# Kernel tuning notes

Measured on AMD Instinct MI355X. Metric: run time of the kernel, lower is better.

The kernel has to match this reference:

```python
import jax, jax.numpy as jnp
import numpy as np

E = 1024
H = 16
HD = E // H
FF = 4 * E
B, T = 2, 2048


def _linear_params(key, fan_in, fan_out):
    k1, k2 = jax.random.split(key)
    bound = 1.0 / np.sqrt(fan_in)
    W = jax.random.uniform(k1, (fan_out, fan_in), jnp.float32, -bound, bound)
    b = jax.random.uniform(k2, (fan_out,), jnp.float32, -bound, bound)
    return W, b


def setup_inputs() -> dict:
    key = jax.random.key(0)
    keys = jax.random.split(key, 8)
    x = jax.random.normal(keys[0], (B, T, E), jnp.float32)
    Wq, bq = _linear_params(keys[1], E, E)
    Wk, bk = _linear_params(keys[2], E, E)
    Wv, bv = _linear_params(keys[3], E, E)
    Wo, bo = _linear_params(keys[4], E, E)
    W1, b1 = _linear_params(keys[5], E, FF)
    W2, b2 = _linear_params(keys[6], FF, E)
    ln1_g = jnp.ones((E,), jnp.float32); ln1_b = jnp.zeros((E,), jnp.float32)
    ln2_g = jnp.ones((E,), jnp.float32); ln2_b = jnp.zeros((E,), jnp.float32)
    return {"x": x, "Wq": Wq, "bq": bq, "Wk": Wk, "bk": bk, "Wv": Wv, "bv": bv,
            "Wo": Wo, "bo": bo, "W1": W1, "b1": b1, "W2": W2, "b2": b2,
            "ln1_g": ln1_g, "ln1_b": ln1_b, "ln2_g": ln2_g, "ln2_b": ln2_b}


def _layernorm(x, g, b, eps=1e-5):
    mu = jnp.mean(x, axis=-1, keepdims=True)
    var = jnp.var(x, axis=-1, keepdims=True)
    return (x - mu) * jax.lax.rsqrt(var + eps) * g + b


def reference(x, Wq, bq, Wk, bk, Wv, bv, Wo, bo, W1, b1, W2, b2,
              ln1_g, ln1_b, ln2_g, ln2_b):
    Bc, Tc, Ec = x.shape
    h = _layernorm(x, ln1_g, ln1_b)
    # projections (torch Linear: y = x @ W.T + b)
    q = (h @ Wq.T + bq).reshape(Bc, Tc, H, HD).transpose(0, 2, 1, 3)  # [B,H,T,hd]
    k = (h @ Wk.T + bk).reshape(Bc, Tc, H, HD).transpose(0, 2, 1, 3)
    v = (h @ Wv.T + bv).reshape(Bc, Tc, H, HD).transpose(0, 2, 1, 3)
    scores = jnp.einsum('bhqd,bhkd->bhqk', q, k) / np.sqrt(HD).astype(np.float32)
    causal = jnp.tril(jnp.ones((Tc, Tc), bool))
    scores = jnp.where(causal, scores, -jnp.inf)
    att = jax.nn.softmax(scores, axis=-1)  # dropout = identity (eval)
    out = jnp.einsum('bhqk,bhkd->bhqd', att, v)
    out = out.transpose(0, 2, 1, 3).reshape(Bc, Tc, Ec)
    x = x + out @ Wo.T + bo
    h2 = _layernorm(x, ln2_g, ln2_b)
    ff = jax.nn.relu(h2 @ W1.T + b1) @ W2.T + b2
    return x + ff
```

## Files before the change

kernel.cpp:

```cpp
#include <hip/hip_runtime.h>

typedef unsigned short u16;
typedef __bf16 bf16x8 __attribute__((ext_vector_type(8)));
typedef float f32x4 __attribute__((ext_vector_type(4)));

#define E_ 1024
#define T_ 2048
#define B_ 2
#define H_ 16
#define FF_ 4096
#define M_ 4096

__device__ __forceinline__ u16 f2b(float f) {
    union { float f; unsigned u; } c; c.f = f;
    unsigned r = c.u + 0x7FFFu + ((c.u >> 16) & 1u);
    return (u16)(r >> 16);
}
__device__ __forceinline__ u16 f2bt(float f) {
    union { float f; unsigned u; } c; c.f = f;
    return (u16)(c.u >> 16);
}

__device__ __forceinline__ void gl16(const u16* g, u16* l) {
    __builtin_amdgcn_global_load_lds(
        (__attribute__((address_space(1))) void*)g,
        (__attribute__((address_space(3))) void*)l, 16, 0, 0);
}

template<int N> __device__ __forceinline__ void wait_vmcnt() {
    if constexpr (N == 2)      asm volatile("s_waitcnt vmcnt(2)" ::: "memory");
    else if constexpr (N == 3) asm volatile("s_waitcnt vmcnt(3)" ::: "memory");
    else if constexpr (N == 4) asm volatile("s_waitcnt vmcnt(4)" ::: "memory");
    else                       asm volatile("s_waitcnt vmcnt(0)" ::: "memory");
}

__global__ __launch_bounds__(256) void cvt_ln(
        const float* __restrict__ Wq, const float* __restrict__ Wk,
        const float* __restrict__ Wv, const float* __restrict__ Wo,
        const float* __restrict__ W1, const float* __restrict__ W2,
        const float* __restrict__ bq, const float* __restrict__ bk,
        const float* __restrict__ bv,
        u16* __restrict__ WqkvB, u16* __restrict__ WoB,
        u16* __restrict__ W1B, u16* __restrict__ W2B,
        float* __restrict__ bqkv,
        const float* __restrict__ x, const float* __restrict__ g1,
        const float* __restrict__ b1v, u16* __restrict__ hB) {
    if (blockIdx.x < 1024) {
        int row = blockIdx.x * 4 + (threadIdx.x >> 6);
        int t = threadIdx.x & 63;
        const float* xr = x + (size_t)row * E_;
        float v[16];
        float sum = 0.f, ss = 0.f;
#pragma unroll
        for (int c = 0; c < 4; c++) {
            float4 f = *(const float4*)&xr[c * 256 + t * 4];
            v[c * 4 + 0] = f.x; v[c * 4 + 1] = f.y; v[c * 4 + 2] = f.z; v[c * 4 + 3] = f.w;
            sum += f.x + f.y + f.z + f.w;
            ss += f.x * f.x + f.y * f.y + f.z * f.z + f.w * f.w;
        }
#pragma unroll
        for (int d = 32; d; d >>= 1) {
            sum += __shfl_xor(sum, d);
            ss  += __shfl_xor(ss, d);
        }
        float mu = sum * (1.f / E_);
        float var = ss * (1.f / E_) - mu * mu;
        float rs = rsqrtf(var + 1e-5f);
#pragma unroll
        for (int c = 0; c < 4; c++) {
            int idx = c * 256 + t * 4;
            float4 g4 = *(const float4*)&g1[idx];
            float4 b4 = *(const float4*)&b1v[idx];
            ushort4 o;
            o.x = f2b((v[c * 4 + 0] - mu) * rs * g4.x + b4.x);
            o.y = f2b((v[c * 4 + 1] - mu) * rs * g4.y + b4.y);
            o.z = f2b((v[c * 4 + 2] - mu) * rs * g4.z + b4.z);
            o.w = f2b((v[c * 4 + 3] - mu) * rs * g4.w + b4.w);
            *(ushort4*)&hB[(size_t)row * E_ + idx] = o;
        }
        return;
    }
    int i = (blockIdx.x - 1024) * 256 + threadIdx.x;
    if (i >= 3146496) return;
    if (i >= 3145728) {
        int j = i - 3145728;
        const float* s = (j < 256) ? bq : (j < 512) ? bk : bv;
        int jj = j & 255;
        *(float4*)&bqkv[j * 4] = *(const float4*)&s[jj * 4];
        return;
    }
    const float* src; u16* dst; int j;
    if (i < 786432) {
        src = (i < 262144) ? Wq : (i < 524288) ? Wk : Wv;
        j = i & 262143;
        dst = WqkvB + (i >> 18) * (E_ * E_);
    } else if (i < 1048576) { j = i - 786432;  src = Wo; dst = WoB; }
    else if (i < 2097152)   { j = i - 1048576; src = W1; dst = W1B; }
    else                    { j = i - 2097152; src = W2; dst = W2B; }
    float4 f = *(const float4*)&src[j * 4];
    ushort4 o;
    o.x = f2b(f.x); o.y = f2b(f.y); o.z = f2b(f.z); o.w = f2b(f.w);
    *(ushort4*)&dst[j * 4] = o;
}

__global__ __launch_bounds__(64) void ln_fwd(u16* __restrict__ out, const float* __restrict__ x,
                                             const float* __restrict__ g, const float* __restrict__ bta) {
    int row = blockIdx.x;
    int t = threadIdx.x;
    const float* xr = x + (size_t)row * E_;
    float v[16];
    float sum = 0.f, ss = 0.f;
#pragma unroll
    for (int c = 0; c < 4; c++) {
        float4 f = *(const float4*)&xr[c * 256 + t * 4];
        v[c * 4 + 0] = f.x; v[c * 4 + 1] = f.y; v[c * 4 + 2] = f.z; v[c * 4 + 3] = f.w;
        sum += f.x + f.y + f.z + f.w;
        ss += f.x * f.x + f.y * f.y + f.z * f.z + f.w * f.w;
    }
#pragma unroll
    for (int d = 32; d; d >>= 1) {
        sum += __shfl_xor(sum, d);
        ss  += __shfl_xor(ss, d);
    }
    float mu = sum * (1.f / E_);
    float var = ss * (1.f / E_) - mu * mu;
    float rs = rsqrtf(var + 1e-5f);
#pragma unroll
    for (int c = 0; c < 4; c++) {
        int idx = c * 256 + t * 4;
        float4 g4 = *(const float4*)&g[idx];
        float4 b4 = *(const float4*)&bta[idx];
        ushort4 o;
        o.x = f2b((v[c * 4 + 0] - mu) * rs * g4.x + b4.x);
        o.y = f2b((v[c * 4 + 1] - mu) * rs * g4.y + b4.y);
        o.z = f2b((v[c * 4 + 2] - mu) * rs * g4.z + b4.z);
        o.w = f2b((v[c * 4 + 3] - mu) * rs * g4.w + b4.w);
        *(ushort4*)&out[(size_t)row * E_ + idx] = o;
    }
}

template<int BM, int BN, int BUFS>
__global__ __launch_bounds__(256) void gemm_bt(
        const u16* __restrict__ A, const u16* __restrict__ Bt,
        const float* __restrict__ bias, const float* __restrict__ residual,
        float* __restrict__ outF, float* __restrict__ oP1,
        float* __restrict__ oP2, float* __restrict__ oP3,
        u16* __restrict__ outB, u16* __restrict__ outVt,
        int M, int N, int K, int ldk, int relu, int qkvmode, int swz) {
    constexpr int MT = BM / 32, NT = BN / 32;
    constexpr int LA = BM / 64, LB = BN / 64;
    __shared__ __align__(16) u16 As[BUFS][BM * 32];
    __shared__ __align__(16) u16 Bs[BUFS][BN * 32];
    int tid = threadIdx.x;
    int bx = blockIdx.x, by = blockIdx.y;
    if (swz) {
        int gx = gridDim.x;
        int nwg = gx * gridDim.y;
        int lin = by * gx + bx;
        int wv = (lin & 7) * (nwg >> 3) + (lin >> 3);
        bx = wv % gx; by = wv / gx;
    }
    int m0 = by * BM, n0 = bx * BN;
    int kz = blockIdx.z;
    int koff = kz * K;
    int wave = tid >> 6, lane = tid & 63;
    int wm = wave & 1, wn = wave >> 1;
    int r16 = lane & 15, kg = lane >> 4;

    const u16* gA = A + (size_t)(m0 + wave * (BM / 4) + (lane >> 2)) * ldk + koff + (lane & 3) * 8;
    const u16* gB = Bt + (size_t)(n0 + wave * (BN / 4) + (lane >> 2)) * ldk + koff + (lane & 3) * 8;
    size_t row16 = (size_t)16 * ldk;
    int aoff = wave * (BM / 4) * 32;
    int boff = wave * (BN / 4) * 32;

    f32x4 acc[MT][NT] = {};

    const int nk = K >> 5;

    auto issue = [&](int kt, int buf) {
        int k1 = kt << 5;
        gl16(gA + k1, As[buf] + aoff);
        if (LA == 2) gl16(gA + k1 + row16, As[buf] + aoff + 512);
        gl16(gB + k1, Bs[buf] + boff);
        if (LB == 2) gl16(gB + k1 + row16, Bs[buf] + boff + 512);
    };

    auto compute = [&](int cb) {
        bf16x8 af[MT], bfr[NT];
#pragma unroll
        for (int mt = 0; mt < MT; mt++)
            af[mt] = *(const bf16x8*)&As[cb][(wm * (BM / 2) + mt * 16 + r16) * 32 + kg * 8];
#pragma unroll
        for (int nt = 0; nt < NT; nt++)
            bfr[nt] = *(const bf16x8*)&Bs[cb][(wn * (BN / 2) + nt * 16 + r16) * 32 + kg * 8];
#pragma unroll
        for (int mt = 0; mt < MT; mt++)
#pragma unroll
            for (int nt = 0; nt < NT; nt++)
                acc[mt][nt] = __builtin_amdgcn_mfma_f32_16x16x32_bf16(af[mt], bfr[nt], acc[mt][nt], 0, 0, 0);
    };

    if constexpr (BUFS == 2) {
        issue(0, 0);
        for (int ks = 0; ks < nk; ks++) {
            __syncthreads();
            if (ks + 1 < nk) issue(ks + 1, (ks + 1) & 1);
            compute(ks & 1);
        }
    } else {
        issue(0, 0);
        issue(1, 1);
        int cur = 0;
        for (int ks = 0; ks < nk - 1; ks++) {
            wait_vmcnt<LA + LB>();
            __builtin_amdgcn_s_barrier();
            asm volatile("" ::: "memory");
            if (ks + 2 < nk) {
                int p2 = cur ? cur - 1 : 2;
                issue(ks + 2, p2);
            }
            compute(cur);
            cur = (cur < 2) ? cur + 1 : 0;
        }
        asm volatile("s_waitcnt vmcnt(0)" ::: "memory");
        __builtin_amdgcn_s_barrier();
        asm volatile("" ::: "memory");
        compute(cur);
    }

#pragma unroll
    for (int mt = 0; mt < MT; mt++) {
#pragma unroll
        for (int nt = 0; nt < NT; nt++) {
            int gm = m0 + wm * (BM / 2) + mt * 16 + kg * 4;
            int gn = n0 + wn * (BN / 2) + nt * 16 + r16;
            float bv = bias[gn];
            if (qkvmode) {
                if (gn < 2048) {
                    float scl = (gn < 1024) ? 0.18033688f : 1.0f;
#pragma unroll
                    for (int r = 0; r < 4; r++)
                        outB[(size_t)(gm + r) * 2048 + gn] = f2b((acc[mt][nt][r] + bv) * scl);
                } else {
                    int bq_ = gm >> 11, tq = gm & 2047, d = gn - 2048;
                    ushort4 ov;
                    ov.x = f2b(acc[mt][nt][0] + bv);
                    ov.y = f2b(acc[mt][nt][1] + bv);
                    ov.z = f2b(acc[mt][nt][2] + bv);
                    ov.w = f2b(acc[mt][nt][3] + bv);
                    *(ushort4*)&outVt[((size_t)(bq_ * 1024 + d)) * 2048 + tq] = ov;
                }
            } else if (oP1) {
                float* po = (kz == 1) ? oP1 : (kz == 2) ? oP2 : oP3;
#pragma unroll
                for (int r = 0; r < 4; r++) {
                    size_t off = (size_t)(gm + r) * N + gn;
                    if (kz == 0) {
                        float v = acc[mt][nt][r] + bv;
                        if (residual) v += residual[off];
                        outF[off] = v;
                    } else {
                        po[off] = acc[mt][nt][r];
                    }
                }
            } else {
#pragma unroll
                for (int r = 0; r < 4; r++) {
                    float v = acc[mt][nt][r] + bv;
                    size_t off = (size_t)(gm + r) * N + gn;
                    if (residual) v += residual[off];
                    if (relu) v = fmaxf(v, 0.f);
                    if (outF) outF[off] = v;
                    else outB[off] = f2b(v);
                }
            }
        }
    }
}

__global__ __launch_bounds__(256) void addf3(float* __restrict__ d, const float* __restrict__ a,
                                             const float* __restrict__ b, const float* __restrict__ c) {
    size_t i = ((size_t)blockIdx.x * 256 + threadIdx.x) * 4;
    float4 vd = *(float4*)&d[i];
    float4 va = *(const float4*)&a[i];
    float4 vb = *(const float4*)&b[i];
    float4 vc = *(const float4*)&c[i];
    vd.x += va.x + vb.x + vc.x;
    vd.y += va.y + vb.y + vc.y;
    vd.z += va.z + vb.z + vc.z;
    vd.w += va.w + vb.w + vc.w;
    *(float4*)&d[i] = vd;
}

#define AST 68
__global__ __launch_bounds__(256) void attn_mfma(
        const u16* __restrict__ qk, const u16* __restrict__ vt,
        u16* __restrict__ out) {
    __shared__ __align__(16) u16 Ks[2][64 * AST];
    __shared__ __align__(16) u16 Vs[2][64 * AST];
    __shared__ __align__(16) u16 Ps[4][16 * AST];

    int bz = blockIdx.x;
    int h  = bz & 15;
    int b  = (bz >> 4) & 1;
    int qt = bz >> 5;

    int tid = threadIdx.x;
    int w = tid >> 6, lane = tid & 63;
    int g = lane >> 4, l16 = lane & 15;

    int qrow = qt * 64 + w * 16 + l16;
    bf16x8 qf[2];
    qf[0] = *(const bf16x8*)&qk[(size_t)(b * T_ + qrow) * 2048 + h * 64 + g * 8];
    qf[1] = *(const bf16x8*)&qk[(size_t)(b * T_ + qrow) * 2048 + h * 64 + 32 + g * 8];

    f32x4 o[4] = {};
    f32x4 lp = {0.f, 0.f, 0.f, 0.f};

    int r1 = tid >> 3, col1 = (tid & 7) * 8;
    const u16* gK = qk + (size_t)(b * T_) * 2048 + 1024 + h * 64;
    const u16* gV = vt + (size_t)(b * 1024 + h * 64) * 2048;

    uint4 kr1 = *(const uint4*)&gK[(size_t)r1 * 2048 + col1];
    uint4 kr2 = *(const uint4*)&gK[(size_t)(r1 + 32) * 2048 + col1];
    uint4 vr1 = *(const uint4*)&gV[(size_t)r1 * 2048 + col1];
    uint4 vr2 = *(const uint4*)&gV[(size_t)(r1 + 32) * 2048 + col1];

    for (int t = 0; t <= qt; t++) {
        int cur = t & 1;
        *(uint4*)&Ks[cur][r1 * AST + col1] = kr1;
        *(uint4*)&Ks[cur][(r1 + 32) * AST + col1] = kr2;
        *(uint4*)&Vs[cur][r1 * AST + col1] = vr1;
        *(uint4*)&Vs[cur][(r1 + 32) * AST + col1] = vr2;
        __syncthreads();
        if (t < qt) {
            int j1 = (t + 1) * 64;
            kr1 = *(const uint4*)&gK[(size_t)(j1 + r1) * 2048 + col1];
            kr2 = *(const uint4*)&gK[(size_t)(j1 + r1 + 32) * 2048 + col1];
            vr1 = *(const uint4*)&gV[(size_t)r1 * 2048 + j1 + col1];
            vr2 = *(const uint4*)&gV[(size_t)(r1 + 32) * 2048 + j1 + col1];
        }

        f32x4 s[4];
#pragma unroll
        for (int nt = 0; nt < 4; nt++) {
            f32x4 c16 = {-16.f, -16.f, -16.f, -16.f};
            bf16x8 k0 = *(const bf16x8*)&Ks[cur][(nt * 16 + l16) * AST + g * 8];
            bf16x8 k1 = *(const bf16x8*)&Ks[cur][(nt * 16 + l16) * AST + 32 + g * 8];
            s[nt] = __builtin_amdgcn_mfma_f32_16x16x32_bf16(qf[0], k0, c16, 0, 0, 0);
            s[nt] = __builtin_amdgcn_mfma_f32_16x16x32_bf16(qf[1], k1, s[nt], 0, 0, 0);
        }

        if (t == qt) {
            int j0 = t * 64;
#pragma unroll
            for (int nt = 0; nt < 4; nt++) {
                int key = j0 + nt * 16 + l16;
#pragma unroll
                for (int r = 0; r < 4; r++) {
                    int q = qt * 64 + w * 16 + g * 4 + r;
                    if (key > q) s[nt][r] = -INFINITY;
                }
            }
        }

#pragma unroll
        for (int nt = 0; nt < 4; nt++)
#pragma unroll
            for (int r = 0; r < 4; r++) {
                float p = exp2f(s[nt][r]);
                lp[r] += p;
                Ps[w][(g * 4 + r) * AST + nt * 16 + l16] = f2bt(p);
            }

#pragma unroll
        for (int kf = 0; kf < 2; kf++) {
            bf16x8 pf = *(const bf16x8*)&Ps[w][l16 * AST + kf * 32 + g * 8];
#pragma unroll
            for (int nt = 0; nt < 4; nt++) {
                bf16x8 vf = *(const bf16x8*)&Vs[cur][(nt * 16 + l16) * AST + kf * 32 + g * 8];
                o[nt] = __builtin_amdgcn_mfma_f32_16x16x32_bf16(pf, vf, o[nt], 0, 0, 0);
            }
        }
    }

#pragma unroll
    for (int x = 1; x <= 8; x <<= 1)
#pragma unroll
        for (int r = 0; r < 4; r++)
            lp[r] += __shfl_xor(lp[r], x);

    float inv[4];
#pragma unroll
    for (int r = 0; r < 4; r++) inv[r] = 1.f / lp[r];
    int qg = qt * 64 + w * 16 + g * 4;
#pragma unroll
    for (int nt = 0; nt < 4; nt++)
#pragma unroll
        for (int r = 0; r < 4; r++)
            out[(size_t)(b * T_ + qg + r) * E_ + h * 64 + nt * 16 + l16] =
                f2b(o[nt][r] * inv[r]);
}

extern "C" void kernel_launch(void* const* d_in, const int* in_sizes, int n_in,
                              void* d_out, int out_size, void* d_ws, size_t ws_size,
                              hipStream_t stream) {
    const float* x    = (const float*)d_in[0];
    const float* Wq   = (const float*)d_in[1];
    const float* bq   = (const float*)d_in[2];
    const float* Wk   = (const float*)d_in[3];
    const float* bk   = (const float*)d_in[4];
    const float* Wv   = (const float*)d_in[5];
    const float* bv   = (const float*)d_in[6];
    const float* Wo   = (const float*)d_in[7];
    const float* bo   = (const float*)d_in[8];
    const float* W1   = (const float*)d_in[9];
    const float* b1   = (const float*)d_in[10];
    const float* W2   = (const float*)d_in[11];
    const float* b2   = (const float*)d_in[12];
    const float* ln1g = (const float*)d_in[13];
    const float* ln1b = (const float*)d_in[14];
    const float* ln2g = (const float*)d_in[15];
    const float* ln2b = (const float*)d_in[16];

    char* ws = (char*)d_ws;
    size_t off = 0;
    auto alloc = [&](size_t bytes) { char* p = ws + off; off += (bytes + 255) & ~(size_t)255; return p; };

    u16*   hB    = (u16*)  alloc((size_t)M_ * E_ * 2);
    u16*   WqkvB = (u16*)  alloc((size_t)3 * E_ * E_ * 2);
    u16*   WoB   = (u16*)  alloc((size_t)E_ * E_ * 2);
    u16*   W1B   = (u16*)  alloc((size_t)FF_ * E_ * 2);
    u16*   W2B   = (u16*)  alloc((size_t)E_ * FF_ * 2);
    float* bqkv  = (float*)alloc(3 * E_ * 4);
    u16*   qkB   = (u16*)  alloc((size_t)M_ * 2 * E_ * 2);
    u16*   vtG   = (u16*)  alloc((size_t)M_ * E_ * 2);
    u16*   attnB = (u16*)  alloc((size_t)M_ * E_ * 2);
    float* x2    = (float*)alloc((size_t)M_ * E_ * 4);
    u16*   h2B   = (u16*)  alloc((size_t)M_ * E_ * 2);
    u16*   rB    = (u16*)  alloc((size_t)M_ * FF_ * 2);
    float* P1    = (float*)alloc((size_t)M_ * E_ * 4);
    float* P2 = (float*)qkB;
    float* P3 = (float*)ws;

    cvt_ln<<<1024 + 12291, 256, 0, stream>>>(Wq, Wk, Wv, Wo, W1, W2, bq, bk, bv,
                                             WqkvB, WoB, W1B, W2B, bqkv,
                                             x, ln1g, ln1b, hB);

    gemm_bt<128, 128, 2><<<dim3(3 * E_ / 128, M_ / 128), 256, 0, stream>>>(
        hB, WqkvB, bqkv, nullptr, nullptr, nullptr, nullptr, nullptr, qkB, vtG,
        M_, 3 * E_, E_, E_, 0, 1, 0);

    attn_mfma<<<B_ * H_ * (T_ / 64), 256, 0, stream>>>(qkB, vtG, attnB);

    gemm_bt<64, 128, 2><<<dim3(E_ / 128, M_ / 64), 256, 0, stream>>>(
        attnB, WoB, bo, x, x2, nullptr, nullptr, nullptr, nullptr, nullptr,
        M_, E_, E_, E_, 0, 0, 0);

    ln_fwd<<<M_, 64, 0, stream>>>(h2B, x2, ln2g, ln2b);

    gemm_bt<128, 128, 2><<<dim3(FF_ / 128, M_ / 128), 256, 0, stream>>>(
        h2B, W1B, b1, nullptr, nullptr, nullptr, nullptr, nullptr, rB, nullptr,
        M_, FF_, E_, E_, 1, 0, 1);

    gemm_bt<128, 128, 2><<<dim3(E_ / 128, M_ / 128, 4), 256, 0, stream>>>(
        rB, W2B, b2, x2, (float*)d_out, P1, P2, P3, nullptr, nullptr,
        M_, E_, FF_ / 4, FF_, 0, 0, 1);

    addf3<<<(M_ * E_) / (256 * 4), 256, 0, stream>>>((float*)d_out, P1, P2, P3);
}
```

Before: 389.1 us.

## Double attention query tile per block and halve FFN2 split-K factor

The attention kernel now has each block handle 128 query rows, with each wave computing two 16-row sub-tiles. Each K/V tile loaded into shared memory is therefore reused twice, and the grid shrinks to half as many blocks. Separately, the second FFN GEMM drops from split-K 4 to split-K 2, so only one partial buffer has to be reduced by a simpler add kernel. The trade-offs are fewer blocks, which makes causal load imbalance worse, a larger register footprint in attention, and lower parallelism in the W2 GEMM.

```diff
diff --git a/kernel.cpp b/kernel.cpp
--- a/kernel.cpp
+++ b/kernel.cpp
@@ -278,18 +278,12 @@
     }
 }
 
-__global__ __launch_bounds__(256) void addf3(float* __restrict__ d, const float* __restrict__ a,
-                                             const float* __restrict__ b, const float* __restrict__ c) {
+__global__ __launch_bounds__(256) void addf1(float* __restrict__ d, const float* __restrict__ p) {
     size_t i = ((size_t)blockIdx.x * 256 + threadIdx.x) * 4;
-    float4 vd = *(float4*)&d[i];
-    float4 va = *(const float4*)&a[i];
-    float4 vb = *(const float4*)&b[i];
-    float4 vc = *(const float4*)&c[i];
-    vd.x += va.x + vb.x + vc.x;
-    vd.y += va.y + vb.y + vc.y;
-    vd.z += va.z + vb.z + vc.z;
-    vd.w += va.w + vb.w + vc.w;
-    *(float4*)&d[i] = vd;
+    float4 a = *(float4*)&d[i];
+    float4 b = *(const float4*)&p[i];
+    a.x += b.x; a.y += b.y; a.z += b.z; a.w += b.w;
+    *(float4*)&d[i] = a;
 }
 
 #define AST 68
@@ -298,24 +292,28 @@
         u16* __restrict__ out) {
     __shared__ __align__(16) u16 Ks[2][64 * AST];
     __shared__ __align__(16) u16 Vs[2][64 * AST];
-    __shared__ __align__(16) u16 Ps[4][16 * AST];
+    __shared__ __align__(16) u16 Ps[4][32 * AST];
 
     int bz = blockIdx.x;
     int h  = bz & 15;
     int b  = (bz >> 4) & 1;
-    int qt = bz >> 5;
+    int q0 = bz >> 5;
 
     int tid = threadIdx.x;
     int w = tid >> 6, lane = tid & 63;
     int g = lane >> 4, l16 = lane & 15;
 
-    int qrow = qt * 64 + w * 16 + l16;
-    bf16x8 qf[2];
-    qf[0] = *(const bf16x8*)&qk[(size_t)(b * T_ + qrow) * 2048 + h * 64 + g * 8];
-    qf[1] = *(const bf16x8*)&qk[(size_t)(b * T_ + qrow) * 2048 + h * 64 + 32 + g * 8];
-
-    f32x4 o[4] = {};
-    f32x4 lp = {0.f, 0.f, 0.f, 0.f};
+    int qbase = q0 * 128 + w * 32;
+    bf16x8 qf[2][2];
+#pragma unroll
+    for (int s = 0; s < 2; s++) {
+        const u16* qp = &qk[(size_t)(b * T_ + qbase + s * 16 + l16) * 2048 + h * 64];
+        qf[s][0] = *(const bf16x8*)&qp[g * 8];
+        qf[s][1] = *(const bf16x8*)&qp[32 + g * 8];
+    }
+
+    f32x4 o[2][4] = {};
+    f32x4 lp[2] = {};
 
     int r1 = tid >> 3, col1 = (tid & 7) * 8;
     const u16* gK = qk + (size_t)(b * T_) * 2048 + 1024 + h * 64;
@@ -326,14 +324,15 @@
     uint4 vr1 = *(const uint4*)&gV[(size_t)r1 * 2048 + col1];
     uint4 vr2 = *(const uint4*)&gV[(size_t)(r1 + 32) * 2048 + col1];
 
-    for (int t = 0; t <= qt; t++) {
+    const int ntiles = 2 * q0 + 2;
+    for (int t = 0; t < ntiles; t++) {
         int cur = t & 1;
         *(uint4*)&Ks[cur][r1 * AST + col1] = kr1;
         *(uint4*)&Ks[cur][(r1 + 32) * AST + col1] = kr2;
         *(uint4*)&Vs[cur][r1 * AST + col1] = vr1;
         *(uint4*)&Vs[cur][(r1 + 32) * AST + col1] = vr2;
         __syncthreads();
-        if (t < qt) {
+        if (t + 1 < ntiles) {
             int j1 = (t + 1) * 64;
             kr1 = *(const uint4*)&gK[(size_t)(j1 + r1) * 2048 + col1];
             kr2 = *(const uint4*)&gK[(size_t)(j1 + r1 + 32) * 2048 + col1];
@@ -341,65 +340,78 @@
             vr2 = *(const uint4*)&gV[(size_t)(r1 + 32) * 2048 + j1 + col1];
         }
 
-        f32x4 s[4];
-#pragma unroll
-        for (int nt = 0; nt < 4; nt++) {
-            f32x4 c16 = {-16.f, -16.f, -16.f, -16.f};
-            bf16x8 k0 = *(const bf16x8*)&Ks[cur][(nt * 16 + l16) * AST + g * 8];
-            bf16x8 k1 = *(const bf16x8*)&Ks[cur][(nt * 16 + l16) * AST + 32 + g * 8];
-            s[nt] = __builtin_amdgcn_mfma_f32_16x16x32_bf16(qf[0], k0, c16, 0, 0, 0);
-            s[nt] = __builtin_amdgcn_mfma_f32_16x16x32_bf16(qf[1], k1, s[nt], 0, 0, 0);
-        }
-
-        if (t == qt) {
-            int j0 = t * 64;
+        const bool diag = (t >= 2 * q0);
+        int j0 = t * 64;
+
+#pragma unroll
+        for (int s = 0; s < 2; s++) {
+            f32x4 sc[4];
 #pragma unroll
             for (int nt = 0; nt < 4; nt++) {
-                int key = j0 + nt * 16 + l16;
+                f32x4 c16 = {-16.f, -16.f, -16.f, -16.f};
+                bf16x8 k0 = *(const bf16x8*)&Ks[cur][(nt * 16 + l16) * AST + g * 8];
+                bf16x8 k1 = *(const bf16x8*)&Ks[cur][(nt * 16 + l16) * AST + 32 + g * 8];
+                sc[nt] = __builtin_amdgcn_mfma_f32_16x16x32_bf16(qf[s][0], k0, c16, 0, 0, 0);
+                sc[nt] = __builtin_amdgcn_mfma_f32_16x16x32_bf16(qf[s][1], k1, sc[nt], 0, 0, 0);
+            }
+
+            if (diag) {
+#pragma unroll
+                for (int nt = 0; nt < 4; nt++) {
+                    int key = j0 + nt * 16 + l16;
+#pragma unroll
+                    for (int r = 0; r < 4; r++) {
+                        int q = qbase + s * 16 + g * 4 + r;
+                        if (key > q) sc[nt][r] = -INFINITY;
+                    }
+                }
+            }
+
+#pragma unroll
+            for (int nt = 0; nt < 4; nt++)
 #pragma unroll
                 for (int r = 0; r < 4; r++) {
-                    int q = qt * 64 + w * 16 + g * 4 + r;
-                    if (key > q) s[nt][r] = -INFINITY;
+                    float p = exp2f(sc[nt][r]);
+                    lp[s][r] += p;
+                    Ps[w][(s * 16 + g * 4 + r) * AST + nt * 16 + l16] = f2bt(p);
+                }
+        }
+
+#pragma unroll
+        for (int s = 0; s < 2; s++) {
+#pragma unroll
+            for (int kf = 0; kf < 2; kf++) {
+                bf16x8 pf = *(const bf16x8*)&Ps[w][(s * 16 + l16) * AST + kf * 32 + g * 8];
+#pragma unroll
+                for (int nt = 0; nt < 4; nt++) {
+                    bf16x8 vf = *(const bf16x8*)&Vs[cur][(nt * 16 + l16) * AST + kf * 32 + g * 8];
+                    o[s][nt] = __builtin_amdgcn_mfma_f32_16x16x32_bf16(pf, vf, o[s][nt], 0, 0, 0);
                 }
             }
         }
-
+    }
+
+#pragma unroll
+    for (int s = 0; s < 2; s++)
+#pragma unroll
+        for (int x = 1; x <= 8; x <<= 1)
+#pragma unroll
+            for (int r = 0; r < 4; r++)
+                lp[s][r] += __shfl_xor(lp[s][r], x);
+
+#pragma unroll
+    for (int s = 0; s < 2; s++) {
+        float inv[4];
+#pragma unroll
+        for (int r = 0; r < 4; r++) inv[r] = 1.f / lp[s][r];
+        int qg = qbase + s * 16 + g * 4;
 #pragma unroll
         for (int nt = 0; nt < 4; nt++)
 #pragma unroll
-            for (int r = 0; r < 4; r++) {
-                float p = exp2f(s[nt][r]);
-                lp[r] += p;
-                Ps[w][(g * 4 + r) * AST + nt * 16 + l16] = f2bt(p);
-            }
-
-#pragma unroll
-        for (int kf = 0; kf < 2; kf++) {
-            bf16x8 pf = *(const bf16x8*)&Ps[w][l16 * AST + kf * 32 + g * 8];
-#pragma unroll
-            for (int nt = 0; nt < 4; nt++) {
-                bf16x8 vf = *(const bf16x8*)&Vs[cur][(nt * 16 + l16) * AST + kf * 32 + g * 8];
-                o[nt] = __builtin_amdgcn_mfma_f32_16x16x32_bf16(pf, vf, o[nt], 0, 0, 0);
-            }
-        }
-    }
-
-#pragma unroll
-    for (int x = 1; x <= 8; x <<= 1)
-#pragma unroll
-        for (int r = 0; r < 4; r++)
-            lp[r] += __shfl_xor(lp[r], x);
-
-    float inv[4];
-#pragma unroll
-    for (int r = 0; r < 4; r++) inv[r] = 1.f / lp[r];
-    int qg = qt * 64 + w * 16 + g * 4;
-#pragma unroll
-    for (int nt = 0; nt < 4; nt++)
-#pragma unroll
-        for (int r = 0; r < 4; r++)
-            out[(size_t)(b * T_ + qg + r) * E_ + h * 64 + nt * 16 + l16] =
-                f2b(o[nt][r] * inv[r]);
+            for (int r = 0; r < 4; r++)
+                out[(size_t)(b * T_ + qg + r) * E_ + h * 64 + nt * 16 + l16] =
+                    f2b(o[s][nt][r] * inv[r]);
+    }
 }
 
 extern "C" void kernel_launch(void* const* d_in, const int* in_sizes, int n_in,
@@ -440,8 +452,6 @@
     u16*   h2B   = (u16*)  alloc((size_t)M_ * E_ * 2);
     u16*   rB    = (u16*)  alloc((size_t)M_ * FF_ * 2);
     float* P1    = (float*)alloc((size_t)M_ * E_ * 4);
-    float* P2 = (float*)qkB;
-    float* P3 = (float*)ws;
 
     cvt_ln<<<1024 + 12291, 256, 0, stream>>>(Wq, Wk, Wv, Wo, W1, W2, bq, bk, bv,
                                              WqkvB, WoB, W1B, W2B, bqkv,
@@ -451,7 +461,7 @@
         hB, WqkvB, bqkv, nullptr, nullptr, nullptr, nullptr, nullptr, qkB, vtG,
         M_, 3 * E_, E_, E_, 0, 1, 0);
 
-    attn_mfma<<<B_ * H_ * (T_ / 64), 256, 0, stream>>>(qkB, vtG, attnB);
+    attn_mfma<<<B_ * H_ * (T_ / 128), 256, 0, stream>>>(qkB, vtG, attnB);
 
     gemm_bt<64, 128, 2><<<dim3(E_ / 128, M_ / 64), 256, 0, stream>>>(
         attnB, WoB, bo, x, x2, nullptr, nullptr, nullptr, nullptr, nullptr,
@@ -463,9 +473,9 @@
         h2B, W1B, b1, nullptr, nullptr, nullptr, nullptr, nullptr, rB, nullptr,
         M_, FF_, E_, E_, 1, 0, 1);
 
-    gemm_bt<128, 128, 2><<<dim3(E_ / 128, M_ / 128, 4), 256, 0, stream>>>(
-        rB, W2B, b2, x2, (float*)d_out, P1, P2, P3, nullptr, nullptr,
-        M_, E_, FF_ / 4, FF_, 0, 0, 1);
-
-    addf3<<<(M_ * E_) / (256 * 4), 256, 0, stream>>>((float*)d_out, P1, P2, P3);
-}
+    gemm_bt<128, 128, 2><<<dim3(E_ / 128, M_ / 128, 2), 256, 0, stream>>>(
+        rB, W2B, b2, x2, (float*)d_out, P1, nullptr, nullptr, nullptr, nullptr,
+        M_, E_, FF_ / 2, FF_, 0, 0, 1);
+
+    addf1<<<(M_ * E_) / (256 * 4), 256, 0, stream>>>((float*)d_out, P1);
+}
```

Result: slower. 406.4 us (+4.4%).
